# Performance work log

Measured on AMD Instinct MI355X. Metric: run time of the kernel, lower is better.

Reference implementation:

```python
import jax, jax.numpy as jnp
import numpy as np

N, C, K = 200000, 128, 27  # active voxels, channels, 3x3x3 kernel taps
EPS = 1e-5  # torch LayerNorm default


def setup_inputs() -> dict:
    key = jax.random.key(0)
    ks = jax.random.split(key, 8)
    feats = jax.random.normal(ks[0], (N, C), dtype=jnp.float32)
    # plan-based gather map: neighbor row index per voxel per kernel tap
    neighbor_idx = jax.random.randint(ks[1], (N, K), 0, N, dtype=jnp.int32)
    # sparse conv weights: one [C_in, C_out] slice per kernel offset
    conv_w = jax.random.normal(ks[2], (K, C, C), dtype=jnp.float32) * (1.0 / np.sqrt(K * C))
    conv_b = jax.random.normal(ks[3], (C,), dtype=jnp.float32) * 0.02
    # torch.nn.Linear(C, C): weight [out, in], y = x @ W^T + b
    lin_w = jax.random.normal(ks[4], (C, C), dtype=jnp.float32) * (1.0 / np.sqrt(C))
    lin_b = jax.random.normal(ks[5], (C,), dtype=jnp.float32) * 0.02
    ln_w = 1.0 + 0.02 * jax.random.normal(ks[6], (C,), dtype=jnp.float32)
    ln_b = 0.02 * jax.random.normal(ks[7], (C,), dtype=jnp.float32)
    return {
        "feats": feats, "neighbor_idx": neighbor_idx,
        "conv_w": conv_w, "conv_b": conv_b,
        "lin_w": lin_w, "lin_b": lin_b,
        "ln_w": ln_w, "ln_b": ln_b,
    }


def _sparse_conv(feats, neighbor_idx, conv_w, conv_b):
    # Stream over the 27 kernel taps: gather [N,C] then GEMM with the tap's
    # [C,C] slice; never materialize the [N,27,C] gathered tensor.
    def step(acc, tap):
        idx_k, w_k = tap  # idx_k: [N], w_k: [C, C]
        return acc + feats[idx_k] @ w_k, None

    acc0 = jnp.zeros((feats.shape[0], conv_w.shape[2]), dtype=feats.dtype)
    out, _ = jax.lax.scan(step, acc0, (neighbor_idx.T, conv_w))
    return out + conv_b


def reference(feats, neighbor_idx, conv_w, conv_b, lin_w, lin_b, ln_w, ln_b):
    x = _sparse_conv(feats, neighbor_idx, conv_w, conv_b)   # [N, C]
    x = x @ lin_w.T + lin_b                                  # Linear
    mu = jnp.mean(x, axis=-1, keepdims=True)                 # LayerNorm
    var = jnp.mean(jnp.square(x - mu), axis=-1, keepdims=True)
    x = (x - mu) * jax.lax.rsqrt(var + EPS) * ln_w + ln_b
    return x
```

## Files before the change

kernel.cpp:

```cpp
#include <hip/hip_runtime.h>
#include <hip/hip_bf16.h>
#include <stdint.h>

#define N_ROWS 200000
#define C_DIM  128
#define TAPS   27
#define EPS    1e-5f

typedef __attribute__((ext_vector_type(8)))  short  short8;
typedef __attribute__((ext_vector_type(16))) float  floatx16;

#if __has_builtin(__builtin_amdgcn_make_buffer_rsrc) && __has_builtin(__builtin_amdgcn_raw_buffer_load_b128)
#define GATHER_SC0 1
#else
#define GATHER_SC0 0
#endif

#define SBAR()  __builtin_amdgcn_s_barrier()
#define SCHED() __builtin_amdgcn_sched_barrier(0)

__device__ __forceinline__ unsigned int f2bf(float f) {
  union { float f; unsigned int u; } v; v.f = f;
  unsigned int r = v.u + 0x7FFFu + ((v.u >> 16) & 1u);
  return r >> 16;
}

__device__ __forceinline__ void glds16(const unsigned short* g, unsigned short* l) {
  __builtin_amdgcn_global_load_lds(
      (const __attribute__((address_space(1))) unsigned int*)g,
      (__attribute__((address_space(3))) unsigned int*)l, 16, 0, 0);
}

#if GATHER_SC0
__device__ __forceinline__ short8 ld16sc0(__amdgpu_buffer_rsrc_t r, int voff) {
  return __builtin_bit_cast(short8,
      __builtin_amdgcn_raw_buffer_load_b128(r, voff, 0, 1));
}
#endif

__global__ __launch_bounds__(256) void k_cast(const float* __restrict__ in,
                                              unsigned short* __restrict__ out, int n8) {
  int i = blockIdx.x * 256 + threadIdx.x;
  if (i >= n8) return;
  const float4* p = (const float4*)in + (size_t)i * 2;
  float4 a = p[0], b = p[1];
  uint4 v;
  v.x = f2bf(a.x) | (f2bf(a.y) << 16);
  v.y = f2bf(a.z) | (f2bf(a.w) << 16);
  v.z = f2bf(b.x) | (f2bf(b.y) << 16);
  v.w = f2bf(b.z) | (f2bf(b.w) << 16);
  *(uint4*)(out + (size_t)i * 8) = v;
}

__global__ __launch_bounds__(256) void k_tr(const int* __restrict__ in,
                                            int* __restrict__ outT) {
  __shared__ int t[1728];
  const int tile = blockIdx.x;
  const int* src = in + (size_t)tile * 1728;
  for (int e = threadIdx.x; e < 1728; e += 256) t[e] = src[e];
  __syncthreads();
  const int base = tile * 64;
  for (int o = threadIdx.x; o < 1728; o += 256) {
    int k = o >> 6, r = o & 63;
    outT[(size_t)k * N_ROWS + base + r] = t[r * 27 + k];
  }
}

__global__ __launch_bounds__(256) void k_fold(const float* __restrict__ conv_w,
                                              const float* __restrict__ lin_w,
                                              const float* __restrict__ conv_b,
                                              const float* __restrict__ lin_b,
                                              unsigned short* __restrict__ wfrag,
                                              float* __restrict__ biasf) {
  __shared__ float lwT[128 * 128];
  for (int e = threadIdx.x; e < 16384; e += 256) {
    int co = e >> 7, t = e & 127;
    lwT[t * 128 + (co ^ (t & 31))] = lin_w[e];
  }
  __syncthreads();

  int id = blockIdx.x * 256 + threadIdx.x;
  const int NW = TAPS * 2 * 4 * 4 * 64;
  if (id < NW) {
    int l  = id & 63;
    int sh = (id >> 6) & 3;
    int nt = (id >> 8) & 3;
    int h  = (id >> 10) & 1;
    int k  = id >> 11;
    int s  = h * 4 + sh;
    int ci0 = s * 16 + (l >> 5) * 8;
    int co  = nt * 32 + (l & 31);
    const float* cw = conv_w + ((size_t)(k * 128 + ci0)) * 128;
    float acc[8] = {0, 0, 0, 0, 0, 0, 0, 0};
    for (int t = 0; t < 128; ++t) {
      float lv = lwT[t * 128 + (co ^ (t & 31))];
#pragma unroll
      for (int j = 0; j < 8; ++j) acc[j] += cw[j * 128 + t] * lv;
    }
    uint4 v;
    v.x = f2bf(acc[0]) | (f2bf(acc[1]) << 16);
    v.y = f2bf(acc[2]) | (f2bf(acc[3]) << 16);
    v.z = f2bf(acc[4]) | (f2bf(acc[5]) << 16);
    v.w = f2bf(acc[6]) | (f2bf(acc[7]) << 16);
    *(uint4*)(wfrag + (size_t)id * 8) = v;
  } else if (id < NW + 128) {
    int co = id - NW;
    float s = lin_b[co];
    for (int t = 0; t < 128; ++t) s += conv_b[t] * lwT[t * 128 + (co ^ (t & 31))];
    biasf[co] = s;
  }
}

__global__ __launch_bounds__(256, 4) void k_main(const unsigned short* __restrict__ featsB,
                                                 const int* __restrict__ ntab,
                                                 const int nrs, const int nts,
                                                 const unsigned short* __restrict__ wfrag,
                                                 const float* __restrict__ biasf,
                                                 const float* __restrict__ lnw,
                                                 const float* __restrict__ lnb,
                                                 float* __restrict__ out) {
  __shared__ unsigned short ldsB[2][8192];

  const int tid = threadIdx.x;
  const int l   = tid & 63;
  const int w   = tid >> 6;
  const int l31 = l & 31;
  const int lh  = l >> 5;
  const int row0w = blockIdx.x * 128 + w * 32;
  const int gr  = row0w + l31;
  const int grc = (gr < N_ROWS) ? gr : 0;
  const int* np = ntab + (size_t)grc * nrs;

#if GATHER_SC0
  __amdgpu_buffer_rsrc_t rsrc = __builtin_amdgcn_make_buffer_rsrc(
      (void*)featsB, (short)0, N_ROWS * C_DIM * 2, 0x00020000);
#endif

  floatx16 acc0 = {0.f}, acc1 = {0.f}, acc2 = {0.f}, acc3 = {0.f};

  {
    const unsigned short* src = wfrag + (size_t)tid * 8;
    unsigned short* dst = &ldsB[0][w * 512];
#pragma unroll
    for (int r = 0; r < 4; ++r) glds16(src + r * 2048, dst + r * 2048);
  }
  int nid = np[0];
  short8 a0, a1, a2, a3, a4, a5, a6, a7;

  for (int t = 0; t < TAPS; ++t) {
    {
      const unsigned short* src = wfrag + (size_t)(2 * t + 1) * 8192 + (size_t)tid * 8;
      unsigned short* dst = &ldsB[1][w * 512];
#pragma unroll
      for (int r = 0; r < 4; ++r) glds16(src + r * 2048, dst + r * 2048);
    }
    SCHED();
    __builtin_amdgcn_s_waitcnt(0xF74);
    SCHED();
    SBAR();
    SCHED();

#if GATHER_SC0
    const int voff = ((int)(unsigned)nid << 8) + (lh << 4);
    a0 = ld16sc0(rsrc, voff);
    a1 = ld16sc0(rsrc, voff + 32);
    a2 = ld16sc0(rsrc, voff + 64);
    a3 = ld16sc0(rsrc, voff + 96);
    a4 = ld16sc0(rsrc, voff + 128);
    a5 = ld16sc0(rsrc, voff + 160);
    a6 = ld16sc0(rsrc, voff + 192);
    a7 = ld16sc0(rsrc, voff + 224);
#else
    const short8* ap = (const short8*)(featsB + (size_t)(unsigned)nid * 128 + lh * 8);
    a0 = ap[0];  a1 = ap[2];  a2 = ap[4];  a3 = ap[6];
    a4 = ap[8];  a5 = ap[10]; a6 = ap[12]; a7 = ap[14];
#endif
    int nid_next = (t + 1 < TAPS) ? np[(t + 1) * nts] : 0;

    {
      const unsigned short* bb = &ldsB[0][l * 8];
#pragma unroll
      for (int sh = 0; sh < 4; ++sh) {
        short8 av = (sh == 0) ? a0 : (sh == 1) ? a1 : (sh == 2) ? a2 : a3;
        short8 b0 = *(const short8*)(bb + (0 * 4 + sh) * 512);
        short8 b1 = *(const short8*)(bb + (1 * 4 + sh) * 512);
        short8 b2 = *(const short8*)(bb + (2 * 4 + sh) * 512);
        short8 b3 = *(const short8*)(bb + (3 * 4 + sh) * 512);
        acc0 = __builtin_amdgcn_mfma_f32_32x32x16_bf16(av, b0, acc0, 0, 0, 0);
        acc1 = __builtin_amdgcn_mfma_f32_32x32x16_bf16(av, b1, acc1, 0, 0, 0);
        acc2 = __builtin_amdgcn_mfma_f32_32x32x16_bf16(av, b2, acc2, 0, 0, 0);
        acc3 = __builtin_amdgcn_mfma_f32_32x32x16_bf16(av, b3, acc3, 0, 0, 0);
      }
    }
    SCHED();
    SBAR();
    SCHED();

    if (t + 1 < TAPS) {
      const unsigned short* src = wfrag + (size_t)(2 * t + 2) * 8192 + (size_t)tid * 8;
      unsigned short* dst = &ldsB[0][w * 512];
#pragma unroll
      for (int r = 0; r < 4; ++r) glds16(src + r * 2048, dst + r * 2048);
    }
    SCHED();
    SBAR();
    SCHED();
    {
      const unsigned short* bb = &ldsB[1][l * 8];
#pragma unroll
      for (int sh = 0; sh < 4; ++sh) {
        short8 av = (sh == 0) ? a4 : (sh == 1) ? a5 : (sh == 2) ? a6 : a7;
        short8 b0 = *(const short8*)(bb + (0 * 4 + sh) * 512);
        short8 b1 = *(const short8*)(bb + (1 * 4 + sh) * 512);
        short8 b2 = *(const short8*)(bb + (2 * 4 + sh) * 512);
        short8 b3 = *(const short8*)(bb + (3 * 4 + sh) * 512);
        acc0 = __builtin_amdgcn_mfma_f32_32x32x16_bf16(av, b0, acc0, 0, 0, 0);
        acc1 = __builtin_amdgcn_mfma_f32_32x32x16_bf16(av, b1, acc1, 0, 0, 0);
        acc2 = __builtin_amdgcn_mfma_f32_32x32x16_bf16(av, b2, acc2, 0, 0, 0);
        acc3 = __builtin_amdgcn_mfma_f32_32x32x16_bf16(av, b3, acc3, 0, 0, 0);
      }
    }
    if (t + 1 < TAPS) {
      SCHED();
      SBAR();
      SCHED();
    }
    nid = nid_next;
  }

  float b0 = biasf[l31], b1 = biasf[32 + l31], b2 = biasf[64 + l31], b3 = biasf[96 + l31];
  float g0 = lnw[l31],   g1 = lnw[32 + l31],   g2 = lnw[64 + l31],   g3 = lnw[96 + l31];
  float c0 = lnb[l31],   c1 = lnb[32 + l31],   c2 = lnb[64 + l31],   c3 = lnb[96 + l31];

#pragma unroll
  for (int r = 0; r < 16; ++r) {
    float x0 = acc0[r] + b0, x1 = acc1[r] + b1, x2 = acc2[r] + b2, x3 = acc3[r] + b3;
    float s = x0 + x1 + x2 + x3;
    float q = x0 * x0 + x1 * x1 + x2 * x2 + x3 * x3;
#pragma unroll
    for (int off = 16; off >= 1; off >>= 1) {
      s += __shfl_xor(s, off, 64);
      q += __shfl_xor(q, off, 64);
    }
    float mu  = s * (1.0f / 128.0f);
    float var = q * (1.0f / 128.0f) - mu * mu;
    float rs  = rsqrtf(var + EPS);
    int row   = (r & 3) + 8 * (r >> 2) + 4 * lh;
    int grow  = row0w + row;
    if (grow < N_ROWS) {
      float* o = out + (size_t)grow * 128;
      o[l31]      = (x0 - mu) * rs * g0 + c0;
      o[32 + l31] = (x1 - mu) * rs * g1 + c1;
      o[64 + l31] = (x2 - mu) * rs * g2 + c2;
      o[96 + l31] = (x3 - mu) * rs * g3 + c3;
    }
  }
}

extern "C" void kernel_launch(void* const* d_in, const int* in_sizes, int n_in,
                              void* d_out, int out_size, void* d_ws, size_t ws_size,
                              hipStream_t stream) {
  const float* feats  = (const float*)d_in[0];
  const int*   nidx   = (const int*)d_in[1];
  const float* conv_w = (const float*)d_in[2];
  const float* conv_b = (const float*)d_in[3];
  const float* lin_w  = (const float*)d_in[4];
  const float* lin_b  = (const float*)d_in[5];
  const float* ln_w   = (const float*)d_in[6];
  const float* ln_b   = (const float*)d_in[7];
  float* out = (float*)d_out;

  unsigned short* featsB = (unsigned short*)d_ws;
  unsigned short* wfrag  = (unsigned short*)((char*)d_ws + 51200000);
  float*          biasf  = (float*)((char*)d_ws + 51200000 + 884736);
  int*            nidxT  = (int*)((char*)d_ws + 51200000 + 884736 + 512);

  const size_t ws_need_tr = 51200000ULL + 884736ULL + 512ULL + 21600000ULL;
  const bool use_tr = (ws_size >= ws_need_tr);

  int n8 = N_ROWS * C_DIM / 8;
  k_cast<<<(n8 + 255) / 256, 256, 0, stream>>>(feats, featsB, n8);
  k_fold<<<(TAPS * 2048 + 128 + 255) / 256, 256, 0, stream>>>(conv_w, lin_w, conv_b, lin_b,
                                                              wfrag, biasf);
  if (use_tr) k_tr<<<N_ROWS / 64, 256, 0, stream>>>(nidx, nidxT);

  k_main<<<(N_ROWS + 127) / 128, 256, 0, stream>>>(
      featsB,
      use_tr ? (const int*)nidxT : nidx,
      use_tr ? 1 : TAPS,
      use_tr ? N_ROWS : 1,
      wfrag, biasf, ln_w, ln_b, out);
}
```

Baseline: 481.0 us.

## Pipeline weight staging in four quarter-tap LDS slots with early feature gathers

```diff
diff --git a/kernel.cpp b/kernel.cpp
--- a/kernel.cpp
+++ b/kernel.cpp
@@ -80,14 +80,14 @@
   __syncthreads();
 
   int id = blockIdx.x * 256 + threadIdx.x;
-  const int NW = TAPS * 2 * 4 * 4 * 64;
+  const int NW = TAPS * 4 * 4 * 2 * 64;
   if (id < NW) {
     int l  = id & 63;
-    int sh = (id >> 6) & 3;
-    int nt = (id >> 8) & 3;
-    int h  = (id >> 10) & 1;
+    int sh = (id >> 6) & 1;
+    int nt = (id >> 7) & 3;
+    int qr = (id >> 9) & 3;
     int k  = id >> 11;
-    int s  = h * 4 + sh;
+    int s  = qr * 2 + sh;
     int ci0 = s * 16 + (l >> 5) * 8;
     int co  = nt * 32 + (l & 31);
     const float* cw = conv_w + ((size_t)(k * 128 + ci0)) * 128;
@@ -119,7 +119,7 @@
                                                  const float* __restrict__ lnw,
                                                  const float* __restrict__ lnb,
                                                  float* __restrict__ out) {
-  __shared__ unsigned short ldsB[2][8192];
+  __shared__ unsigned short lds4[4][4096];
 
   const int tid = threadIdx.x;
   const int l   = tid & 63;
@@ -134,98 +134,116 @@
 #if GATHER_SC0
   __amdgpu_buffer_rsrc_t rsrc = __builtin_amdgcn_make_buffer_rsrc(
       (void*)featsB, (short)0, N_ROWS * C_DIM * 2, 0x00020000);
+#define A_LD(vo) ld16sc0(rsrc, (vo))
+#else
+#define A_LD(vo) (*(const short8*)((const char*)featsB + (vo)))
 #endif
 
+#define STAGE(Qi, slot) do {                                                 \
+    int Qc = (Qi) > 4 * TAPS - 1 ? 4 * TAPS - 1 : (Qi);                      \
+    const unsigned short* s_ = wfrag + (size_t)Qc * 4096 + tid * 8;          \
+    unsigned short* d_ = &lds4[slot][w * 512];                               \
+    glds16(s_, d_);                                                          \
+    glds16(s_ + 2048, d_ + 2048);                                            \
+  } while (0)
+
+#define COMPQ(slot, avA, avB) do {                                           \
+    const unsigned short* bb = &lds4[slot][l * 8];                           \
+    short8 c0 = *(const short8*)(bb + 0);                                    \
+    short8 c1 = *(const short8*)(bb + 1024);                                 \
+    short8 c2 = *(const short8*)(bb + 2048);                                 \
+    short8 c3 = *(const short8*)(bb + 3072);                                 \
+    acc0 = __builtin_amdgcn_mfma_f32_32x32x16_bf16(avA, c0, acc0, 0, 0, 0);  \
+    acc1 = __builtin_amdgcn_mfma_f32_32x32x16_bf16(avA, c1, acc1, 0, 0, 0);  \
+    acc2 = __builtin_amdgcn_mfma_f32_32x32x16_bf16(avA, c2, acc2, 0, 0, 0);  \
+    acc3 = __builtin_amdgcn_mfma_f32_32x32x16_bf16(avA, c3, acc3, 0, 0, 0);  \
+    short8 d0 = *(const short8*)(bb + 512);                                  \
+    short8 d1 = *(const short8*)(bb + 1536);                                 \
+    short8 d2 = *(const short8*)(bb + 2560);                                 \
+    short8 d3 = *(const short8*)(bb + 3584);                                 \
+    acc0 = __builtin_amdgcn_mfma_f32_32x32x16_bf16(avB, d0, acc0, 0, 0, 0);  \
+    acc1 = __builtin_amdgcn_mfma_f32_32x32x16_bf16(avB, d1, acc1, 0, 0, 0);  \
+    acc2 = __builtin_amdgcn_mfma_f32_32x32x16_bf16(avB, d2, acc2, 0, 0, 0);  \
+    acc3 = __builtin_amdgcn_mfma_f32_32x32x16_bf16(avB, d3, acc3, 0, 0, 0);  \
+  } while (0)
+
   floatx16 acc0 = {0.f}, acc1 = {0.f}, acc2 = {0.f}, acc3 = {0.f};
 
+  STAGE(0, 0);
+  STAGE(1, 1);
+  STAGE(2, 2);
+  int nid_cur = np[0];
+  int nid_nxt = np[nts];
+  int nid_fut;
+  __builtin_amdgcn_s_waitcnt(0xF70);
+  SCHED();
+  short8 a0, a1, a2, a3, a4, a5, a6, a7;
   {
-    const unsigned short* src = wfrag + (size_t)tid * 8;
-    unsigned short* dst = &ldsB[0][w * 512];
-#pragma unroll
-    for (int r = 0; r < 4; ++r) glds16(src + r * 2048, dst + r * 2048);
-  }
-  int nid = np[0];
-  short8 a0, a1, a2, a3, a4, a5, a6, a7;
+    const int vo = ((int)(unsigned)nid_cur << 8) + (lh << 4);
+    a0 = A_LD(vo);
+    a1 = A_LD(vo + 32);
+    a2 = A_LD(vo + 64);
+    a3 = A_LD(vo + 96);
+    a4 = A_LD(vo + 128);
+    a5 = A_LD(vo + 160);
+  }
+  SCHED();
 
   for (int t = 0; t < TAPS; ++t) {
+    if (t == 0) __builtin_amdgcn_s_waitcnt(0xF74);
+    else        __builtin_amdgcn_s_waitcnt(0xF78);
+    SCHED(); SBAR(); SCHED();
     {
-      const unsigned short* src = wfrag + (size_t)(2 * t + 1) * 8192 + (size_t)tid * 8;
-      unsigned short* dst = &ldsB[1][w * 512];
-#pragma unroll
-      for (int r = 0; r < 4; ++r) glds16(src + r * 2048, dst + r * 2048);
-    }
-    SCHED();
-    __builtin_amdgcn_s_waitcnt(0xF74);
-    SCHED();
-    SBAR();
-    SCHED();
-
-#if GATHER_SC0
-    const int voff = ((int)(unsigned)nid << 8) + (lh << 4);
-    a0 = ld16sc0(rsrc, voff);
-    a1 = ld16sc0(rsrc, voff + 32);
-    a2 = ld16sc0(rsrc, voff + 64);
-    a3 = ld16sc0(rsrc, voff + 96);
-    a4 = ld16sc0(rsrc, voff + 128);
-    a5 = ld16sc0(rsrc, voff + 160);
-    a6 = ld16sc0(rsrc, voff + 192);
-    a7 = ld16sc0(rsrc, voff + 224);
-#else
-    const short8* ap = (const short8*)(featsB + (size_t)(unsigned)nid * 128 + lh * 8);
-    a0 = ap[0];  a1 = ap[2];  a2 = ap[4];  a3 = ap[6];
-    a4 = ap[8];  a5 = ap[10]; a6 = ap[12]; a7 = ap[14];
-#endif
-    int nid_next = (t + 1 < TAPS) ? np[(t + 1) * nts] : 0;
-
+      const int tf = (t + 2 < TAPS) ? (t + 2) : (TAPS - 1);
+      nid_fut = np[(size_t)tf * nts];
+      const int vo = ((int)(unsigned)nid_cur << 8) + (lh << 4);
+      a6 = A_LD(vo + 192);
+      a7 = A_LD(vo + 224);
+    }
+    SCHED();
+    STAGE(4 * t + 3, 3);
+    SCHED();
+    COMPQ(0, a0, a1);
+
+    if (t == 0) __builtin_amdgcn_s_waitcnt(0xF77);
+    else        __builtin_amdgcn_s_waitcnt(0xF79);
+    SCHED(); SBAR(); SCHED();
     {
-      const unsigned short* bb = &ldsB[0][l * 8];
-#pragma unroll
-      for (int sh = 0; sh < 4; ++sh) {
-        short8 av = (sh == 0) ? a0 : (sh == 1) ? a1 : (sh == 2) ? a2 : a3;
-        short8 b0 = *(const short8*)(bb + (0 * 4 + sh) * 512);
-        short8 b1 = *(const short8*)(bb + (1 * 4 + sh) * 512);
-        short8 b2 = *(const short8*)(bb + (2 * 4 + sh) * 512);
-        short8 b3 = *(const short8*)(bb + (3 * 4 + sh) * 512);
-        acc0 = __builtin_amdgcn_mfma_f32_32x32x16_bf16(av, b0, acc0, 0, 0, 0);
-        acc1 = __builtin_amdgcn_mfma_f32_32x32x16_bf16(av, b1, acc1, 0, 0, 0);
-        acc2 = __builtin_amdgcn_mfma_f32_32x32x16_bf16(av, b2, acc2, 0, 0, 0);
-        acc3 = __builtin_amdgcn_mfma_f32_32x32x16_bf16(av, b3, acc3, 0, 0, 0);
-      }
-    }
-    SCHED();
-    SBAR();
-    SCHED();
-
-    if (t + 1 < TAPS) {
-      const unsigned short* src = wfrag + (size_t)(2 * t + 2) * 8192 + (size_t)tid * 8;
-      unsigned short* dst = &ldsB[0][w * 512];
-#pragma unroll
-      for (int r = 0; r < 4; ++r) glds16(src + r * 2048, dst + r * 2048);
-    }
-    SCHED();
-    SBAR();
-    SCHED();
+      const int vo = ((int)(unsigned)nid_nxt << 8) + (lh << 4);
+      a0 = A_LD(vo);
+      a1 = A_LD(vo + 32);
+    }
+    SCHED();
+    STAGE(4 * t + 4, 0);
+    SCHED();
+    COMPQ(1, a2, a3);
+
+    __builtin_amdgcn_s_waitcnt(0xF79);
+    SCHED(); SBAR(); SCHED();
     {
-      const unsigned short* bb = &ldsB[1][l * 8];
-#pragma unroll
-      for (int sh = 0; sh < 4; ++sh) {
-        short8 av = (sh == 0) ? a4 : (sh == 1) ? a5 : (sh == 2) ? a6 : a7;
-        short8 b0 = *(const short8*)(bb + (0 * 4 + sh) * 512);
-        short8 b1 = *(const short8*)(bb + (1 * 4 + sh) * 512);
-        short8 b2 = *(const short8*)(bb + (2 * 4 + sh) * 512);
-        short8 b3 = *(const short8*)(bb + (3 * 4 + sh) * 512);
-        acc0 = __builtin_amdgcn_mfma_f32_32x32x16_bf16(av, b0, acc0, 0, 0, 0);
-        acc1 = __builtin_amdgcn_mfma_f32_32x32x16_bf16(av, b1, acc1, 0, 0, 0);
-        acc2 = __builtin_amdgcn_mfma_f32_32x32x16_bf16(av, b2, acc2, 0, 0, 0);
-        acc3 = __builtin_amdgcn_mfma_f32_32x32x16_bf16(av, b3, acc3, 0, 0, 0);
-      }
-    }
-    if (t + 1 < TAPS) {
-      SCHED();
-      SBAR();
-      SCHED();
-    }
-    nid = nid_next;
+      const int vo = ((int)(unsigned)nid_nxt << 8) + (lh << 4);
+      a2 = A_LD(vo + 64);
+      a3 = A_LD(vo + 96);
+    }
+    SCHED();
+    STAGE(4 * t + 5, 1);
+    SCHED();
+    COMPQ(2, a4, a5);
+
+    __builtin_amdgcn_s_waitcnt(0xF78);
+    SCHED(); SBAR(); SCHED();
+    {
+      const int vo = ((int)(unsigned)nid_nxt << 8) + (lh << 4);
+      a4 = A_LD(vo + 128);
+      a5 = A_LD(vo + 160);
+    }
+    SCHED();
+    STAGE(4 * t + 6, 2);
+    SCHED();
+    COMPQ(3, a6, a7);
+
+    nid_cur = nid_nxt;
+    nid_nxt = nid_fut;
   }
 
   float b0 = biasf[l31], b1 = biasf[32 + l31], b2 = biasf[64 + l31], b3 = biasf[96 + l31];
```

Result: no change. 483.4 us (+0.5%).
